# Performance work log

Hardware: AMD Instinct MI355X
Metric: run time of the kernel (lower is better)

The kernel has to match this reference:

```python
import jax, jax.numpy as jnp
import numpy as np

D = 2048    # d_model (feature_dimm)
H = 8       # n_heads
P = 4       # n_points (n_levels = 1)
NL = 4      # num_encoder_layers
DFF = 2048  # dim_feedforward
BS = 2
T = 2048


def setup_inputs() -> dict:
    key = jax.random.key(0)
    ks = jax.random.split(key, 10)
    s = 0.02
    def w(k, shape):
        return jax.random.normal(k, shape, jnp.float32) * s
    return {
        "src": jax.random.normal(ks[0], (BS, D, T), jnp.float32),
        "mask": jnp.ones((BS, T), dtype=bool),
        "level_embed": w(ks[1], (1, D)),
        "Wo": w(ks[2], (NL, D, H * P)), "bo": jnp.zeros((NL, H * P), jnp.float32),
        "Wa": w(ks[3], (NL, D, H * P)), "ba": jnp.zeros((NL, H * P), jnp.float32),
        "Wv": w(ks[4], (NL, D, D)), "bv": jnp.zeros((NL, D), jnp.float32),
        "Wout": w(ks[5], (NL, D, D)), "bout": jnp.zeros((NL, D), jnp.float32),
        "ln1_g": jnp.ones((NL, D), jnp.float32), "ln1_b": jnp.zeros((NL, D), jnp.float32),
        "W1": w(ks[6], (NL, D, DFF)), "b1": jnp.zeros((NL, DFF), jnp.float32),
        "W2": w(ks[7], (NL, DFF, D)), "b2": jnp.zeros((NL, D), jnp.float32),
        "ln2_g": jnp.ones((NL, D), jnp.float32), "ln2_b": jnp.zeros((NL, D), jnp.float32),
    }


def _layer_norm(x, g, b):
    mu = jnp.mean(x, axis=-1, keepdims=True)
    var = jnp.mean((x - mu) ** 2, axis=-1, keepdims=True)
    return (x - mu) * jax.lax.rsqrt(var + 1e-5) * g + b


def _pos_embed_sine(mask, d):
    # 1D PositionEmbeddingSine, normalize=True, temperature=10000
    bs, t = mask.shape
    emb = jnp.cumsum(mask.astype(jnp.float32), axis=1)
    emb = emb / (emb[:, -1:] + 1e-6) * jnp.float32(2.0 * np.pi)
    dim_t = 10000.0 ** (2.0 * (jnp.arange(d) // 2).astype(jnp.float32) / d)
    pos = emb[:, :, None] / dim_t  # (bs, t, d)
    pos = jnp.stack([jnp.sin(pos[..., 0::2]), jnp.cos(pos[..., 1::2])], axis=3)
    return pos.reshape(bs, t, d)


def _deform_attn(q, src, ref, Wv, bv, Wo, bo, Wa, ba, Wout, bout):
    # 1D multi-scale deformable attention, single level.
    bs, Q, d = q.shape
    T_ = src.shape[1]
    dh = d // H
    value = (src @ Wv + bv).reshape(bs, T_, H, dh)
    off = (q @ Wo + bo).reshape(bs, Q, H, P)
    attn = jax.nn.softmax((q @ Wa + ba).reshape(bs, Q, H, P), axis=-1)
    # normalized sampling locations in [0, 1]
    loc = ref[:, :, 0, 0][:, :, None, None] + off / T_  # (bs, Q, H, P)
    x = loc * T_ - 0.5
    i0 = jnp.floor(x)
    w1 = x - i0
    i0i = i0.astype(jnp.int32)
    i1i = i0i + 1
    v0 = ((i0i >= 0) & (i0i < T_)).astype(jnp.float32)  # zero padding
    v1 = ((i1i >= 0) & (i1i < T_)).astype(jnp.float32)
    i0c = jnp.clip(i0i, 0, T_ - 1)
    i1c = jnp.clip(i1i, 0, T_ - 1)
    vh = value.transpose(0, 2, 1, 3)  # (bs, H, T, dh)
    def gather(idx):  # idx: (bs, Q, H, P) -> (bs, H, Q, P, dh)
        idxh = idx.transpose(0, 2, 1, 3).reshape(bs, H, Q * P)
        g = jnp.take_along_axis(vh, idxh[:, :, :, None], axis=2)
        return g.reshape(bs, H, Q, P, dh)
    w0m = ((1.0 - w1) * v0).transpose(0, 2, 1, 3)  # (bs, H, Q, P)
    w1m = (w1 * v1).transpose(0, 2, 1, 3)
    sampled = gather(i0c) * w0m[..., None] + gather(i1c) * w1m[..., None]
    out = jnp.einsum('bhqp,bhqpd->bhqd', attn.transpose(0, 2, 1, 3), sampled)
    out = out.transpose(0, 2, 1, 3).reshape(bs, Q, d)
    return out @ Wout + bout


def reference(src, mask, level_embed, Wo, bo, Wa, ba, Wv, bv, Wout, bout,
              ln1_g, ln1_b, W1, b1, W2, b2, ln2_g, ln2_b):
    bs, c, t = src.shape
    pos = _pos_embed_sine(mask, c)          # (bs, t, c)
    x = src.transpose(0, 2, 1)              # (bs, t, c)
    lvl_pos = pos + level_embed             # (1, c) broadcasts
    vr = jnp.sum(mask.astype(jnp.float32), axis=1) / t  # valid ratios (bs,)
    ref = jnp.linspace(0.5, t - 0.5, t, dtype=jnp.float32)[None] / (vr[:, None] * t)
    ref = (ref * vr[:, None])[:, :, None, None]  # (bs, t, 1, 1)
    for i in range(NL):
        q = x + lvl_pos
        a = _deform_attn(q, x, ref, Wv[i], bv[i], Wo[i], bo[i], Wa[i], ba[i], Wout[i], bout[i])
        x = _layer_norm(x + a, ln1_g[i], ln1_b[i])
        h = jax.nn.relu(x @ W1[i] + b1[i]) @ W2[i] + b2[i]
        x = _layer_norm(x + h, ln2_g[i], ln2_b[i])
    return (x.transpose(0, 2, 1), mask[:, None])
```

## Files before the change

### kernel.cpp

```cpp
#include <hip/hip_runtime.h>

typedef unsigned int u32;
typedef unsigned short u16;
typedef short s8v __attribute__((ext_vector_type(8)));
typedef float f4v __attribute__((ext_vector_type(4)));

#define D_ 2048
#define T_ 2048
#define BS_ 2
#define H_ 8
#define P_ 4
#define NL_ 4
#define DFF_ 2048
#define LDK_ 2048
#define TBUF 24576

#define AS1 __attribute__((address_space(1)))
#define AS3 __attribute__((address_space(3)))

static __device__ __forceinline__ u16 f2bf(float f) {
    u32 u = __float_as_uint(f);
    u = (u + 0x7FFFu + ((u >> 16) & 1u)) >> 16;
    return (u16)u;
}
static __device__ __forceinline__ float bf2f(u16 v) {
    return __uint_as_float(((u32)v) << 16);
}

__global__ void pos_k(const float* __restrict__ le, u16* __restrict__ posbf) {
    int t = blockIdx.x;
    float scale = ((float)(t + 1)) / (2048.0f + 1e-6f) * 6.283185307179586f;
    for (int d = threadIdx.x; d < D_; d += 256) {
        int k = d >> 1;
        float inv_dt = expf(-(float)k * 0.008994473019508361f);
        float th = scale * inv_dt;
        float v = (d & 1) ? cosf(th) : sinf(th);
        posbf[(size_t)t * D_ + d] = f2bf(v + le[d]);
    }
}

__global__ __launch_bounds__(256) void transpose_src_k(const float* __restrict__ src,
                                                       float* __restrict__ x,
                                                       u16* __restrict__ xbf) {
    __shared__ float tile[64][65];
    int b = blockIdx.z;
    int t0 = blockIdx.x * 64, d0 = blockIdx.y * 64;
    const float* s = src + (size_t)b * D_ * T_;
#pragma unroll
    for (int p = 0; p < 16; ++p) {
        int idx = threadIdx.x + p * 256;
        int r = idx >> 6, c = idx & 63;
        tile[r][c] = s[(size_t)(d0 + r) * T_ + t0 + c];
    }
    __syncthreads();
    float* xb = x + (size_t)b * T_ * D_;
    u16* xbb = xbf + (size_t)b * T_ * D_;
#pragma unroll
    for (int p = 0; p < 16; ++p) {
        int idx = threadIdx.x + p * 256;
        int r = idx >> 6, c = idx & 63;
        float v = tile[c][r];
        size_t o = (size_t)(t0 + r) * D_ + d0 + c;
        xb[o] = v;
        xbb[o] = f2bf(v);
    }
}

__global__ __launch_bounds__(256) void transpose_out_k(const float* __restrict__ x,
                                                       float* __restrict__ outp) {
    __shared__ float tile[64][65];
    int b = blockIdx.z;
    int t0 = blockIdx.x * 64, d0 = blockIdx.y * 64;
    const float* xb = x + (size_t)b * T_ * D_;
#pragma unroll
    for (int p = 0; p < 16; ++p) {
        int idx = threadIdx.x + p * 256;
        int r = idx >> 6, c = idx & 63;
        tile[r][c] = xb[(size_t)(t0 + r) * D_ + d0 + c];
    }
    __syncthreads();
    float* ob = outp + (size_t)b * D_ * T_;
#pragma unroll
    for (int p = 0; p < 16; ++p) {
        int idx = threadIdx.x + p * 256;
        int r = idx >> 6, c = idx & 63;
        ob[(size_t)(d0 + r) * T_ + t0 + c] = tile[c][r];
    }
}

__global__ void mask_out_k(float* __restrict__ outp) {
    int i = blockIdx.x * 256 + threadIdx.x;
    if (i < BS_ * T_) outp[i] = 1.0f;
}

__global__ __launch_bounds__(256) void transpose_cvt4_k(const float* __restrict__ Wv,
                                                        const float* __restrict__ Wout,
                                                        const float* __restrict__ W1,
                                                        const float* __restrict__ W2,
                                                        u16* __restrict__ WtV,
                                                        u16* __restrict__ Wt1,
                                                        u16* __restrict__ Wt2,
                                                        u16* __restrict__ Wt3) {
    __shared__ float tile[64][65];
    int z = blockIdx.z;
    const float* W = (z == 0) ? Wv : (z == 1) ? Wout : (z == 2) ? W1 : W2;
    u16* Wt = (z == 0) ? WtV : (z == 1) ? Wt1 : (z == 2) ? Wt2 : Wt3;
    int k0 = blockIdx.x * 64, n0 = blockIdx.y * 64;
#pragma unroll
    for (int p = 0; p < 16; ++p) {
        int idx = threadIdx.x + p * 256;
        int r = idx >> 6, c = idx & 63;
        tile[r][c] = W[(size_t)(k0 + r) * 2048 + n0 + c];
    }
    __syncthreads();
#pragma unroll
    for (int p = 0; p < 16; ++p) {
        int idx = threadIdx.x + p * 256;
        int r = idx >> 6, c = idx & 63;
        Wt[(size_t)(n0 + r) * 2048 + k0 + c] = f2bf(tile[c][r]);
    }
}

__global__ void build_qtall_k(const float* __restrict__ Wo, const float* __restrict__ Wa,
                              const float* __restrict__ bo, const float* __restrict__ ba,
                              u16* __restrict__ WqtAll, float* __restrict__ bqaAll) {
    int i = blockIdx.x * 256 + threadIdx.x;
    int l = i >> 18;
    int rem = i & 262143;
    int n = rem >> 11, k = rem & 2047;
    float v = 0.f;
    if (n < 32) v = Wo[((size_t)l * 2048 + k) * 32 + n];
    else if (n < 64) v = Wa[((size_t)l * 2048 + k) * 32 + (n - 32)];
    WqtAll[i] = f2bf(v);
    if (i < NL_ * 128) {
        int ll = i >> 7, nn = i & 127;
        float bb = 0.f;
        if (nn < 32) bb = bo[ll * 32 + nn];
        else if (nn < 64) bb = ba[ll * 32 + (nn - 32)];
        bqaAll[i] = bb;
    }
}

static __device__ __forceinline__ void stage6(const u16* __restrict__ As,
                                              const u16* __restrict__ Bs,
                                              u16* lbuf, int w, int k0) {
#pragma unroll
    for (int s = 0; s < 4; ++s) {
        int seg = s * 8 + w;
        __builtin_amdgcn_global_load_lds((AS1 void*)(As + (size_t)(seg * 8) * LDK_ + k0),
                                         (AS3 void*)(lbuf + seg * 512), 16, 0, 0);
    }
#pragma unroll
    for (int s = 0; s < 2; ++s) {
        int seg = s * 8 + w;
        __builtin_amdgcn_global_load_lds((AS1 void*)(Bs + (size_t)(seg * 8) * LDK_ + k0),
                                         (AS3 void*)(lbuf + 16384 + seg * 512), 16, 0, 0);
    }
}

static __device__ __forceinline__ void gemm_core256(const u16* __restrict__ A,
                                                    const u16* __restrict__ Bt,
                                                    int bm, int bn, int kbase, int kext,
                                                    u16* lds, f4v (&acc)[4][4]) {
    int tid = threadIdx.x;
    int w = tid >> 6, lane = tid & 63;
    int quad = lane >> 4, lrow = lane & 15;
    int wr = w >> 1, wc = w & 1;
    int srow = lane >> 3;
    int sg = (lane & 7) ^ srow;
    const u16* As = A + (size_t)(bm * 256 + srow) * LDK_ + kbase + sg * 8;
    const u16* Bs = Bt + (size_t)(bn * 128 + srow) * LDK_ + kbase + sg * 8;
    int nt = kext >> 6;

    stage6(As, Bs, lds, w, 0);
    stage6(As, Bs, lds + TBUF, w, 64);
    int cur = 0, nxt = 2;
    for (int t = 0; t < nt; ++t) {
        if (t != nt - 1)
            asm volatile("s_waitcnt vmcnt(6)" ::: "memory");
        else
            asm volatile("s_waitcnt vmcnt(0)" ::: "memory");
        __builtin_amdgcn_s_barrier();
        __builtin_amdgcn_sched_barrier(0);
        if (t + 2 < nt) stage6(As, Bs, lds + nxt * TBUF, w, (t + 2) << 6);
        const u16* lA = lds + cur * TBUF;
        const u16* lB = lA + 16384;

        s8v af[2][2], bfr[4][2];
#pragma unroll
        for (int i = 0; i < 2; ++i) {
            int r = wr * 64 + i * 16 + lrow;
#pragma unroll
            for (int c = 0; c < 2; ++c)
                af[i][c] = *(const s8v*)&lA[r * 64 + (((c * 4 + quad) ^ (r & 7)) * 8)];
        }
#pragma unroll
        for (int j = 0; j < 4; ++j) {
            int r = wc * 64 + j * 16 + lrow;
#pragma unroll
            for (int c = 0; c < 2; ++c)
                bfr[j][c] = *(const s8v*)&lB[r * 64 + (((c * 4 + quad) ^ (r & 7)) * 8)];
        }
        __builtin_amdgcn_s_setprio(1);
#pragma unroll
        for (int c = 0; c < 2; ++c)
#pragma unroll
            for (int i = 0; i < 2; ++i)
#pragma unroll
                for (int j = 0; j < 4; ++j)
                    acc[i][j] = __builtin_amdgcn_mfma_f32_16x16x32_bf16(af[i][c], bfr[j][c],
                                                                       acc[i][j], 0, 0, 0);
        __builtin_amdgcn_s_setprio(0);
#pragma unroll
        for (int i = 0; i < 2; ++i) {
            int r = wr * 64 + (i + 2) * 16 + lrow;
#pragma unroll
            for (int c = 0; c < 2; ++c)
                af[i][c] = *(const s8v*)&lA[r * 64 + (((c * 4 + quad) ^ (r & 7)) * 8)];
        }
        __builtin_amdgcn_s_setprio(1);
#pragma unroll
        for (int c = 0; c < 2; ++c)
#pragma unroll
            for (int i = 0; i < 2; ++i)
#pragma unroll
                for (int j = 0; j < 4; ++j)
                    acc[i + 2][j] = __builtin_amdgcn_mfma_f32_16x16x32_bf16(af[i][c], bfr[j][c],
                                                                            acc[i + 2][j], 0, 0, 0);
        __builtin_amdgcn_s_setprio(0);
        cur = (cur == 2) ? 0 : cur + 1;
        nxt = (nxt == 2) ? 0 : nxt + 1;
    }
}

static __device__ __forceinline__ void store_bf_ep(u16* __restrict__ C, int N, int row0, int col0,
                                                   const float* __restrict__ bias, int relu,
                                                   f4v (&acc)[4][4], int quad, int lrow) {
#pragma unroll
    for (int j = 0; j < 4; ++j) {
        int col = col0 + j * 16 + lrow;
        float bcol = bias[col];
#pragma unroll
        for (int i = 0; i < 4; ++i) {
            int rbase = row0 + i * 16 + quad * 4;
#pragma unroll
            for (int r = 0; r < 4; ++r) {
                float vv = acc[i][j][r] + bcol;
                if (relu) vv = fmaxf(vv, 0.f);
                C[(size_t)(rbase + r) * N + col] = f2bf(vv);
            }
        }
    }
}

__global__ __launch_bounds__(512, 2) void gemm_f32_256(const u16* __restrict__ A,
                                                       const u16* __restrict__ Bt,
                                                       const float* __restrict__ bias,
                                                       float* __restrict__ C, int N) {
    __shared__ u16 lds[3 * TBUF];
    f4v acc[4][4] = {};
    gemm_core256(A, Bt, blockIdx.x, blockIdx.y, 0, LDK_, lds, acc);
    int tid = threadIdx.x, w = tid >> 6, lane = tid & 63;
    int quad = lane >> 4, lrow = lane & 15, wr = w >> 1, wc = w & 1;
    int row0 = blockIdx.x * 256 + wr * 64;
    int col0 = blockIdx.y * 128 + wc * 64;
#pragma unroll
    for (int j = 0; j < 4; ++j) {
        int col = col0 + j * 16 + lrow;
        float bcol = bias[col];
#pragma unroll
        for (int i = 0; i < 4; ++i) {
            int rbase = row0 + i * 16 + quad * 4;
#pragma unroll
            for (int r = 0; r < 4; ++r)
                C[(size_t)(rbase + r) * N + col] = acc[i][j][r] + bcol;
        }
    }
}

__global__ __launch_bounds__(512, 2) void gemm_bf256(const u16* __restrict__ A,
                                                     const u16* __restrict__ Bt,
                                                     const float* __restrict__ bias,
                                                     u16* __restrict__ C,
                                                     int N, int relu) {
    __shared__ u16 lds[3 * TBUF];
    f4v acc[4][4] = {};
    int f = blockIdx.x;
    int xcd = f & 7, local = f >> 3;
    int bm = xcd * 2 + (local & 1);
    int bn = local >> 1;
    gemm_core256(A, Bt, bm, bn, 0, LDK_, lds, acc);
    int tid = threadIdx.x, w = tid >> 6, lane = tid & 63;
    int quad = lane >> 4, lrow = lane & 15, wr = w >> 1, wc = w & 1;
    store_bf_ep(C, N, bm * 256 + wr * 64, bn * 128 + wc * 64, bias, relu, acc, quad, lrow);
}

__global__ __launch_bounds__(512, 2) void gemm_vq256(const u16* __restrict__ A,
                                                     const u16* __restrict__ WtV,
                                                     const u16* __restrict__ WtQ,
                                                     const float* __restrict__ bv,
                                                     u16* __restrict__ value,
                                                     float* __restrict__ smp) {
    __shared__ u16 lds[3 * TBUF];
    f4v acc[4][4] = {};
    int f = blockIdx.x;
    int tid = threadIdx.x, w = tid >> 6, lane = tid & 63;
    int quad = lane >> 4, lrow = lane & 15, wr = w >> 1, wc = w & 1;
    if (f >= 128) {
        int g = f - 128;
        int xcd = g & 7, local = g >> 3;
        int bm = xcd * 2 + (local & 1);
        int bn = local >> 1;
        gemm_core256(A, WtV, bm, bn, 0, LDK_, lds, acc);
        store_bf_ep(value, 2048, bm * 256 + wr * 64, bn * 128 + wc * 64, bv, 0, acc, quad, lrow);
    } else {
        int ks = f >> 4;
        int bm = f & 15;
        gemm_core256(A, WtQ, bm, 0, ks * 256, 256, lds, acc);
        if (wc == 0) {
            int row0 = bm * 256 + wr * 64;
            float* sp = smp + (size_t)ks * (4096 * 64);
#pragma unroll
            for (int j = 0; j < 4; ++j) {
                int col = j * 16 + lrow;
#pragma unroll
                for (int i = 0; i < 4; ++i) {
                    int rbase = row0 + i * 16 + quad * 4;
#pragma unroll
                    for (int r = 0; r < 4; ++r)
                        sp[(size_t)(rbase + r) * 64 + col] = acc[i][j][r];
                }
            }
        }
    }
}

__global__ __launch_bounds__(256) void sampler_k(const u16* __restrict__ value,
                                                 const float* __restrict__ smp,
                                                 const float* __restrict__ Ppos,
                                                 int loff,
                                                 u16* __restrict__ abf) {
    int bq = blockIdx.x;
    int qi = bq & (T_ - 1);
    int b = bq >> 11;
    __shared__ float s[64];
    if (threadIdx.x < 64) {
        float v = Ppos[(size_t)qi * (NL_ * 128) + loff + threadIdx.x];
        const float* sp = smp + (size_t)bq * 64 + threadIdx.x;
#pragma unroll
        for (int ks = 0; ks < 8; ++ks) v += sp[(size_t)ks * (4096 * 64)];
        s[threadIdx.x] = v;
    }
    __syncthreads();
    int head = threadIdx.x >> 5;
    int c8 = (threadIdx.x & 31) * 8;
    const u16* vb = value + (size_t)b * T_ * D_ + head * 256 + c8;

    float l0 = s[32 + head * 4 + 0], l1 = s[32 + head * 4 + 1];
    float l2 = s[32 + head * 4 + 2], l3 = s[32 + head * 4 + 3];
    float mx = fmaxf(fmaxf(l0, l1), fmaxf(l2, l3));
    float e0 = __expf(l0 - mx), e1 = __expf(l1 - mx);
    float e2 = __expf(l2 - mx), e3 = __expf(l3 - mx);
    float inv = 1.f / (e0 + e1 + e2 + e3);
    float at[4] = {e0 * inv, e1 * inv, e2 * inv, e3 * inv};

    float o[8] = {};
#pragma unroll
    for (int p = 0; p < 4; ++p) {
        float xp = (float)qi + s[head * 4 + p];
        float fl = floorf(xp);
        float w1 = xp - fl;
        int i0 = (int)fl;
        int i1 = i0 + 1;
        float w0m = (i0 >= 0 && i0 < T_) ? (1.f - w1) : 0.f;
        float w1m = (i1 >= 0 && i1 < T_) ? w1 : 0.f;
        int i0c = min(max(i0, 0), T_ - 1);
        int i1c = min(max(i1, 0), T_ - 1);
        s8v v0 = *(const s8v*)(vb + (size_t)i0c * D_);
        s8v v1 = *(const s8v*)(vb + (size_t)i1c * D_);
        float a = at[p];
#pragma unroll
        for (int e = 0; e < 8; ++e)
            o[e] += a * (w0m * bf2f((u16)v0[e]) + w1m * bf2f((u16)v1[e]));
    }
    s8v ov;
#pragma unroll
    for (int e = 0; e < 8; ++e) ov[e] = (short)f2bf(o[e]);
    *(s8v*)(abf + (size_t)bq * D_ + head * 256 + c8) = ov;
}

__global__ __launch_bounds__(256) void resid_ln_k(const float* __restrict__ xin,
                                                  const u16* __restrict__ res,
                                                  const float* __restrict__ g,
                                                  const float* __restrict__ be,
                                                  float* __restrict__ xout,
                                                  u16* __restrict__ xbf) {
    int row = blockIdx.x;
    int base = threadIdx.x * 8;
    const float* xr = xin + (size_t)row * D_ + base;
    const u16* rr = res + (size_t)row * D_ + base;
    f4v x0 = *(const f4v*)xr;
    f4v x1 = *(const f4v*)(xr + 4);
    s8v rv = *(const s8v*)rr;
    float v[8];
#pragma unroll
    for (int i = 0; i < 4; ++i) v[i] = x0[i] + bf2f((u16)rv[i]);
#pragma unroll
    for (int i = 0; i < 4; ++i) v[4 + i] = x1[i] + bf2f((u16)rv[4 + i]);
    float s = 0.f, ss = 0.f;
#pragma unroll
    for (int i = 0; i < 8; ++i) { s += v[i]; ss += v[i] * v[i]; }
#pragma unroll
    for (int o = 32; o > 0; o >>= 1) {
        s += __shfl_down(s, o, 64);
        ss += __shfl_down(ss, o, 64);
    }
    __shared__ float w1s[4], w2s[4];
    int wid = threadIdx.x >> 6, lane = threadIdx.x & 63;
    if (lane == 0) { w1s[wid] = s; w2s[wid] = ss; }
    __syncthreads();
    s = w1s[0] + w1s[1] + w1s[2] + w1s[3];
    ss = w2s[0] + w2s[1] + w2s[2] + w2s[3];
    float mu = s * (1.f / 2048.f);
    float var = ss * (1.f / 2048.f) - mu * mu;
    float rinv = rsqrtf(var + 1e-5f);
    f4v g0 = *(const f4v*)(g + base);
    f4v g1 = *(const f4v*)(g + base + 4);
    f4v b0 = *(const f4v*)(be + base);
    f4v b1 = *(const f4v*)(be + base + 4);
    f4v y0, y1;
    s8v yb;
#pragma unroll
    for (int i = 0; i < 4; ++i) {
        float y = (v[i] - mu) * rinv * g0[i] + b0[i];
        y0[i] = y;
        yb[i] = (short)f2bf(y);
    }
#pragma unroll
    for (int i = 0; i < 4; ++i) {
        float y = (v[4 + i] - mu) * rinv * g1[i] + b1[i];
        y1[i] = y;
        yb[4 + i] = (short)f2bf(y);
    }
    float* xo = xout + (size_t)row * D_ + base;
    *(f4v*)xo = y0;
    *(f4v*)(xo + 4) = y1;
    *(s8v*)(xbf + (size_t)row * D_ + base) = yb;
}

extern "C" void kernel_launch(void* const* d_in, const int* in_sizes, int n_in,
                              void* d_out, int out_size, void* d_ws, size_t ws_size,
                              hipStream_t stream) {
    const float* src = (const float*)d_in[0];
    const float* level_embed = (const float*)d_in[2];
    const float* Wo = (const float*)d_in[3];
    const float* bo = (const float*)d_in[4];
    const float* Wa = (const float*)d_in[5];
    const float* ba = (const float*)d_in[6];
    const float* Wv = (const float*)d_in[7];
    const float* bv = (const float*)d_in[8];
    const float* Wout = (const float*)d_in[9];
    const float* bout = (const float*)d_in[10];
    const float* ln1_g = (const float*)d_in[11];
    const float* ln1_b = (const float*)d_in[12];
    const float* W1 = (const float*)d_in[13];
    const float* b1 = (const float*)d_in[14];
    const float* W2 = (const float*)d_in[15];
    const float* b2 = (const float*)d_in[16];
    const float* ln2_g = (const float*)d_in[17];
    const float* ln2_b = (const float*)d_in[18];
    float* outp = (float*)d_out;

    char* p = (char*)d_ws;
    auto alloc = [&](size_t bytes) {
        char* r = p;
        p += (bytes + 255) & ~(size_t)255;
        return r;
    };
    const size_t BTD = (size_t)BS_ * T_ * D_;
    float* B_x = (float*)alloc(BTD * 4);
    u16* B_xbf = (u16*)alloc(BTD * 2);
    u16* B_res = (u16*)alloc(BTD * 2);
    u16* B_val = (u16*)alloc(BTD * 2);
    u16* B_h = (u16*)alloc(BTD * 2);
    float* B_smp = (float*)alloc((size_t)8 * 4096 * 64 * 4);
    u16* B_posbf = (u16*)alloc((size_t)T_ * D_ * 2);
    u16* WtV = (u16*)alloc((size_t)D_ * D_ * 2);
    u16* Wt1 = (u16*)alloc((size_t)D_ * D_ * 2);
    u16* Wt2 = (u16*)alloc((size_t)D_ * DFF_ * 2);
    u16* Wt3 = (u16*)alloc((size_t)DFF_ * D_ * 2);
    u16* WqtAll = (u16*)alloc((size_t)NL_ * 128 * D_ * 2);
    float* bqaAll = (float*)alloc(NL_ * 128 * 4);
    float* Ppos = (float*)alloc((size_t)T_ * NL_ * 128 * 4);

    const int M = BS_ * T_;
    dim3 blk(256);
    dim3 gT(T_ / 64, D_ / 64, BS_);
    dim3 gW4(D_ / 64, D_ / 64, 4);

    pos_k<<<T_, blk, 0, stream>>>(level_embed, B_posbf);
    transpose_src_k<<<gT, blk, 0, stream>>>(src, B_x, B_xbf);
    build_qtall_k<<<(NL_ * 128 * D_) / 256, blk, 0, stream>>>(Wo, Wa, bo, ba, WqtAll, bqaAll);
    gemm_f32_256<<<dim3(T_ / 256, NL_ * 128 / 128), dim3(512), 0, stream>>>(
        B_posbf, WqtAll, bqaAll, Ppos, NL_ * 128);

    for (int l = 0; l < NL_; ++l) {
        transpose_cvt4_k<<<gW4, blk, 0, stream>>>(
            Wv + (size_t)l * D_ * D_, Wout + (size_t)l * D_ * D_,
            W1 + (size_t)l * D_ * DFF_, W2 + (size_t)l * DFF_ * D_,
            WtV, Wt1, Wt2, Wt3);

        gemm_vq256<<<384, dim3(512), 0, stream>>>(B_xbf, WtV, WqtAll + (size_t)l * 128 * D_,
                                                  bv + l * D_, B_val, B_smp);
        sampler_k<<<M, blk, 0, stream>>>(B_val, B_smp, Ppos, l * 128, B_h);
        gemm_bf256<<<256, dim3(512), 0, stream>>>(B_h, Wt1, bout + l * D_, B_res, D_, 0);
        resid_ln_k<<<M, blk, 0, stream>>>(B_x, B_res, ln1_g + l * D_, ln1_b + l * D_, B_x, B_xbf);
        gemm_bf256<<<256, dim3(512), 0, stream>>>(B_xbf, Wt2, b1 + l * DFF_, B_h, DFF_, 1);
        gemm_bf256<<<256, dim3(512), 0, stream>>>(B_h, Wt3, b2 + l * D_, B_res, D_, 0);
        resid_ln_k<<<M, blk, 0, stream>>>(B_x, B_res, ln2_g + l * D_, ln2_b + l * D_, B_x, B_xbf);
    }

    transpose_out_k<<<gT, blk, 0, stream>>>(B_x, outp);
    mask_out_k<<<(BS_ * T_ + 255) / 256, blk, 0, stream>>>(outp + BTD);
}
```

Baseline: 1.172 ms.

## Merge preprocessing kernels and split-K the positional projection GEMM

Folds the positional-embedding, projection-weight packing and source-transpose kernels into one launch, and folds the mask fill into the output transpose. The positional offset/attention projection GEMM now runs split-K over four partitions (128 blocks instead of 32), so it fills more compute units. The sampler sums the four partial results and adds the bias itself. This removes several launches and the underfilled GEMM, in exchange for extra partial-sum traffic in every sampler call.

```diff
diff --git a/kernel.cpp b/kernel.cpp
--- a/kernel.cpp
+++ b/kernel.cpp
@@ -27,42 +27,69 @@
     return __uint_as_float(((u32)v) << 16);
 }
 
-__global__ void pos_k(const float* __restrict__ le, u16* __restrict__ posbf) {
-    int t = blockIdx.x;
-    float scale = ((float)(t + 1)) / (2048.0f + 1e-6f) * 6.283185307179586f;
-    for (int d = threadIdx.x; d < D_; d += 256) {
-        int k = d >> 1;
-        float inv_dt = expf(-(float)k * 0.008994473019508361f);
-        float th = scale * inv_dt;
-        float v = (d & 1) ? cosf(th) : sinf(th);
-        posbf[(size_t)t * D_ + d] = f2bf(v + le[d]);
-    }
-}
-
-__global__ __launch_bounds__(256) void transpose_src_k(const float* __restrict__ src,
-                                                       float* __restrict__ x,
-                                                       u16* __restrict__ xbf) {
+__global__ __launch_bounds__(256) void pre_k(const float* __restrict__ le,
+                                             u16* __restrict__ posbf,
+                                             const float* __restrict__ Wo,
+                                             const float* __restrict__ Wa,
+                                             const float* __restrict__ bo,
+                                             const float* __restrict__ ba,
+                                             u16* __restrict__ WqtAll,
+                                             float* __restrict__ bqaAll,
+                                             const float* __restrict__ src,
+                                             float* __restrict__ x,
+                                             u16* __restrict__ xbf) {
     __shared__ float tile[64][65];
-    int b = blockIdx.z;
-    int t0 = blockIdx.x * 64, d0 = blockIdx.y * 64;
-    const float* s = src + (size_t)b * D_ * T_;
-#pragma unroll
-    for (int p = 0; p < 16; ++p) {
-        int idx = threadIdx.x + p * 256;
-        int r = idx >> 6, c = idx & 63;
-        tile[r][c] = s[(size_t)(d0 + r) * T_ + t0 + c];
-    }
-    __syncthreads();
-    float* xb = x + (size_t)b * T_ * D_;
-    u16* xbb = xbf + (size_t)b * T_ * D_;
-#pragma unroll
-    for (int p = 0; p < 16; ++p) {
-        int idx = threadIdx.x + p * 256;
-        int r = idx >> 6, c = idx & 63;
-        float v = tile[c][r];
-        size_t o = (size_t)(t0 + r) * D_ + d0 + c;
-        xb[o] = v;
-        xbb[o] = f2bf(v);
+    int blk = blockIdx.x;
+    if (blk < T_) {
+        int t = blk;
+        float scale = ((float)(t + 1)) / (2048.0f + 1e-6f) * 6.283185307179586f;
+        for (int d = threadIdx.x; d < D_; d += 256) {
+            int k = d >> 1;
+            float inv_dt = expf(-(float)k * 0.008994473019508361f);
+            float th = scale * inv_dt;
+            float v = (d & 1) ? cosf(th) : sinf(th);
+            posbf[(size_t)t * D_ + d] = f2bf(v + le[d]);
+        }
+    } else if (blk < 6144) {
+        int i = (blk - 2048) * 256 + threadIdx.x;
+        int l = i >> 18;
+        int rem = i & 262143;
+        int n = rem >> 11, k = rem & 2047;
+        float v = 0.f;
+        if (n < 32) v = Wo[((size_t)l * 2048 + k) * 32 + n];
+        else if (n < 64) v = Wa[((size_t)l * 2048 + k) * 32 + (n - 32)];
+        WqtAll[i] = f2bf(v);
+        if (i < NL_ * 128) {
+            int ll = i >> 7, nn = i & 127;
+            float bb = 0.f;
+            if (nn < 32) bb = bo[ll * 32 + nn];
+            else if (nn < 64) bb = ba[ll * 32 + (nn - 32)];
+            bqaAll[i] = bb;
+        }
+    } else {
+        int tt = blk - 6144;
+        int b = tt >> 10;
+        int rem = tt & 1023;
+        int t0 = (rem & 31) * 64, d0 = (rem >> 5) * 64;
+        const float* s = src + (size_t)b * D_ * T_;
+#pragma unroll
+        for (int p = 0; p < 16; ++p) {
+            int idx = threadIdx.x + p * 256;
+            int r = idx >> 6, c = idx & 63;
+            tile[r][c] = s[(size_t)(d0 + r) * T_ + t0 + c];
+        }
+        __syncthreads();
+        float* xb = x + (size_t)b * T_ * D_;
+        u16* xbb = xbf + (size_t)b * T_ * D_;
+#pragma unroll
+        for (int p = 0; p < 16; ++p) {
+            int idx = threadIdx.x + p * 256;
+            int r = idx >> 6, c = idx & 63;
+            float v = tile[c][r];
+            size_t o = (size_t)(t0 + r) * D_ + d0 + c;
+            xb[o] = v;
+            xbb[o] = f2bf(v);
+        }
     }
 }
 
@@ -86,11 +113,11 @@
         int r = idx >> 6, c = idx & 63;
         ob[(size_t)(d0 + r) * T_ + t0 + c] = tile[c][r];
     }
-}
-
-__global__ void mask_out_k(float* __restrict__ outp) {
-    int i = blockIdx.x * 256 + threadIdx.x;
-    if (i < BS_ * T_) outp[i] = 1.0f;
+    if (blockIdx.x == 0 && blockIdx.y == 0) {
+        float* mp = outp + (size_t)BS_ * D_ * T_ + (size_t)b * T_;
+#pragma unroll
+        for (int p = 0; p < 8; ++p) mp[threadIdx.x + p * 256] = 1.0f;
+    }
 }
 
 __global__ __launch_bounds__(256) void transpose_cvt4_k(const float* __restrict__ Wv,
@@ -121,26 +148,6 @@
     }
 }
 
-__global__ void build_qtall_k(const float* __restrict__ Wo, const float* __restrict__ Wa,
-                              const float* __restrict__ bo, const float* __restrict__ ba,
-                              u16* __restrict__ WqtAll, float* __restrict__ bqaAll) {
-    int i = blockIdx.x * 256 + threadIdx.x;
-    int l = i >> 18;
-    int rem = i & 262143;
-    int n = rem >> 11, k = rem & 2047;
-    float v = 0.f;
-    if (n < 32) v = Wo[((size_t)l * 2048 + k) * 32 + n];
-    else if (n < 64) v = Wa[((size_t)l * 2048 + k) * 32 + (n - 32)];
-    WqtAll[i] = f2bf(v);
-    if (i < NL_ * 128) {
-        int ll = i >> 7, nn = i & 127;
-        float bb = 0.f;
-        if (nn < 32) bb = bo[ll * 32 + nn];
-        else if (nn < 64) bb = ba[ll * 32 + (nn - 32)];
-        bqaAll[i] = bb;
-    }
-}
-
 static __device__ __forceinline__ void stage6(const u16* __restrict__ As,
                                               const u16* __restrict__ Bs,
                                               u16* lbuf, int w, int k0) {
@@ -253,27 +260,31 @@
     }
 }
 
-__global__ __launch_bounds__(512, 2) void gemm_f32_256(const u16* __restrict__ A,
-                                                       const u16* __restrict__ Bt,
-                                                       const float* __restrict__ bias,
-                                                       float* __restrict__ C, int N) {
+__global__ __launch_bounds__(512, 2) void gemm_pp(const u16* __restrict__ A,
+                                                  const u16* __restrict__ Bt,
+                                                  float* __restrict__ Cp) {
     __shared__ u16 lds[3 * TBUF];
     f4v acc[4][4] = {};
-    gemm_core256(A, Bt, blockIdx.x, blockIdx.y, 0, LDK_, lds, acc);
+    int f = blockIdx.x;
+    int ks = f >> 5;
+    int rem = f & 31;
+    int bm = rem >> 2;
+    int bn = rem & 3;
+    gemm_core256(A, Bt, bm, bn, ks * 512, 512, lds, acc);
     int tid = threadIdx.x, w = tid >> 6, lane = tid & 63;
     int quad = lane >> 4, lrow = lane & 15, wr = w >> 1, wc = w & 1;
-    int row0 = blockIdx.x * 256 + wr * 64;
-    int col0 = blockIdx.y * 128 + wc * 64;
+    int row0 = bm * 256 + wr * 64;
+    int col0 = bn * 128 + wc * 64;
+    float* Cb = Cp + (size_t)ks * (2048 * 512);
 #pragma unroll
     for (int j = 0; j < 4; ++j) {
         int col = col0 + j * 16 + lrow;
-        float bcol = bias[col];
 #pragma unroll
         for (int i = 0; i < 4; ++i) {
             int rbase = row0 + i * 16 + quad * 4;
 #pragma unroll
             for (int r = 0; r < 4; ++r)
-                C[(size_t)(rbase + r) * N + col] = acc[i][j][r] + bcol;
+                Cb[(size_t)(rbase + r) * 512 + col] = acc[i][j][r];
         }
     }
 }
@@ -337,7 +348,8 @@
 
 __global__ __launch_bounds__(256) void sampler_k(const u16* __restrict__ value,
                                                  const float* __restrict__ smp,
-                                                 const float* __restrict__ Ppos,
+                                                 const float* __restrict__ PposP,
+                                                 const float* __restrict__ bqa,
                                                  int loff,
                                                  u16* __restrict__ abf) {
     int bq = blockIdx.x;
@@ -345,7 +357,10 @@
     int b = bq >> 11;
     __shared__ float s[64];
     if (threadIdx.x < 64) {
-        float v = Ppos[(size_t)qi * (NL_ * 128) + loff + threadIdx.x];
+        float v = bqa[threadIdx.x];
+        const float* pp = PposP + (size_t)qi * 512 + loff + threadIdx.x;
+#pragma unroll
+        for (int ks = 0; ks < 4; ++ks) v += pp[(size_t)ks * (2048 * 512)];
         const float* sp = smp + (size_t)bq * 64 + threadIdx.x;
 #pragma unroll
         for (int ks = 0; ks < 8; ++ks) v += sp[(size_t)ks * (4096 * 64)];
@@ -491,18 +506,16 @@
     u16* Wt3 = (u16*)alloc((size_t)DFF_ * D_ * 2);
     u16* WqtAll = (u16*)alloc((size_t)NL_ * 128 * D_ * 2);
     float* bqaAll = (float*)alloc(NL_ * 128 * 4);
-    float* Ppos = (float*)alloc((size_t)T_ * NL_ * 128 * 4);
+    float* B_PposP = (float*)alloc((size_t)4 * 2048 * 512 * 4);
 
     const int M = BS_ * T_;
     dim3 blk(256);
     dim3 gT(T_ / 64, D_ / 64, BS_);
     dim3 gW4(D_ / 64, D_ / 64, 4);
 
-    pos_k<<<T_, blk, 0, stream>>>(level_embed, B_posbf);
-    transpose_src_k<<<gT, blk, 0, stream>>>(src, B_x, B_xbf);
-    build_qtall_k<<<(NL_ * 128 * D_) / 256, blk, 0, stream>>>(Wo, Wa, bo, ba, WqtAll, bqaAll);
-    gemm_f32_256<<<dim3(T_ / 256, NL_ * 128 / 128), dim3(512), 0, stream>>>(
-        B_posbf, WqtAll, bqaAll, Ppos, NL_ * 128);
+    pre_k<<<8192, blk, 0, stream>>>(level_embed, B_posbf, Wo, Wa, bo, ba,
+                                    WqtAll, bqaAll, src, B_x, B_xbf);
+    gemm_pp<<<128, dim3(512), 0, stream>>>(B_posbf, WqtAll, B_PposP);
 
     for (int l = 0; l < NL_; ++l) {
         transpose_cvt4_k<<<gW4, blk, 0, stream>>>(
@@ -512,7 +525,7 @@
 
         gemm_vq256<<<384, dim3(512), 0, stream>>>(B_xbf, WtV, WqtAll + (size_t)l * 128 * D_,
                                                   bv + l * D_, B_val, B_smp);
-        sampler_k<<<M, blk, 0, stream>>>(B_val, B_smp, Ppos, l * 128, B_h);
+        sampler_k<<<M, blk, 0, stream>>>(B_val, B_smp, B_PposP, bqaAll + l * 128, l * 128, B_h);
         gemm_bf256<<<256, dim3(512), 0, stream>>>(B_h, Wt1, bout + l * D_, B_res, D_, 0);
         resid_ln_k<<<M, blk, 0, stream>>>(B_x, B_res, ln1_g + l * D_, ln1_b + l * D_, B_x, B_xbf);
         gemm_bf256<<<256, dim3(512), 0, stream>>>(B_xbf, Wt2, b1 + l * DFF_, B_h, DFF_, 1);
@@ -521,5 +534,4 @@
     }
 
     transpose_out_k<<<gT, blk, 0, stream>>>(B_x, outp);
-    mask_out_k<<<(BS_ * T_ + 255) / 256, blk, 0, stream>>>(outp + BTD);
-}
+}
```

After: 1.159 ms. Within noise of the previous version (-1.1%).
